# Kernel tuning notes

Measured on AMD Instinct MI355X. Metric: run time of the kernel, lower is better.

## Reference

```python
import jax, jax.numpy as jnp
import numpy as np

B, N, K, EMB, OUT = 16, 1024, 20, 1024, 40
EPS = 1e-5  # BatchNorm eps; eval mode with running_mean=0, running_var=1


def _bn(x, g, b):
    # inference-mode batchnorm (running_mean=0, running_var=1) over channel axis 1
    shp = [1] * x.ndim
    shp[1] = x.shape[1]
    inv = 1.0 / jnp.sqrt(1.0 + EPS)
    return x * inv * g.reshape(shp) + b.reshape(shp)


def _lrelu(v):
    return jnp.where(v >= 0, v, 0.2 * v)


def _knn(x, k):
    # x: (B, C, N) -> (B, N, k) indices of k nearest neighbours
    inner = -2.0 * jnp.einsum('bcn,bcm->bnm', x, x)
    xx = jnp.sum(x * x, axis=1)  # (B, N)
    pd = -xx[:, :, None] - inner - xx[:, None, :]  # negative squared distance
    return jax.lax.top_k(pd, k)[1]


def _graph_feature(x, k):
    # x: (B, C, N) -> (B, 2C, N, k) edge features [x_j - x_i, x_i]
    idx = _knn(x, k)                          # (B, N, k)
    xt = jnp.transpose(x, (0, 2, 1))          # (B, N, C)
    feat = jax.vmap(lambda pts, ind: pts[ind])(xt, idx)  # (B, N, k, C)
    ctr = xt[:, :, None, :]                   # (B, N, 1, C)
    out = jnp.concatenate([feat - ctr, jnp.broadcast_to(ctr, feat.shape)], axis=3)
    return jnp.transpose(out, (0, 3, 1, 2))   # (B, 2C, N, k)


def _local_frames(x, k):
    # x: (B, 3, N) -> (B, 6, N, k); eigh-based local frame + topk gather (no_grad in torch)
    B_, _, N_ = x.shape
    diff = jnp.transpose(x[:, :, None, :] - x[:, :, :, None], (0, 2, 1, 3))  # (B,N,3,N): y[b,i,c,j]=x[b,c,j]-x[b,c,i]
    cov = jnp.einsum('bncm,bndm->bncd', diff, diff)  # (B,N,3,3)
    _, vecs = jnp.linalg.eigh(cov)
    y = jnp.einsum('bndc,bndm->bncm', vecs, diff)    # eigvecs^T @ diff, (B,N,3,N)
    diag = jnp.transpose(jnp.diagonal(y, axis1=1, axis2=3), (0, 2, 1))  # (B,N,3) = y[b,n,:,n]
    y_sub = y - diag[:, :, :, None]
    red = jnp.sum(y_sub * y_sub, axis=2)             # (B,N,N)
    idx = jax.lax.top_k(red, k)[1]                   # (B,N,k) largest
    idxe = jnp.broadcast_to(idx[:, :, None, :], (B_, N_, 3, k))
    gy = jnp.take_along_axis(y, idxe, axis=3)
    gs = jnp.take_along_axis(y_sub, idxe, axis=3)
    x0 = jnp.concatenate([gy, gs], axis=2)           # (B,N,6,k)
    return jnp.transpose(x0, (0, 2, 1, 3))           # (B,6,N,k)


def setup_inputs() -> dict:
    key = jax.random.key(0)
    ks = jax.random.split(key, 30)
    rn = lambda k_, s, sc=0.05: jax.random.normal(k_, s, jnp.float32) * sc
    gm = lambda k_, c: 1.0 + 0.1 * jax.random.normal(k_, (c,), jnp.float32)
    bt = lambda k_, c: 0.1 * jax.random.normal(k_, (c,), jnp.float32)
    return {
        'x': jax.random.normal(ks[0], (B, 3, N), jnp.float32),
        'w1': rn(ks[1], (64, 6)),    'g1': gm(ks[2], 64),  'b1': bt(ks[3], 64),
        'w2': rn(ks[4], (64, 128)),  'g2': gm(ks[5], 64),  'b2': bt(ks[6], 64),
        'w3': rn(ks[7], (128, 128)), 'g3': gm(ks[8], 128), 'b3': bt(ks[9], 128),
        'w4': rn(ks[10], (256, 256)),'g4': gm(ks[11], 256),'b4': bt(ks[12], 256),
        'w5': rn(ks[13], (EMB, 512)),'g5': gm(ks[14], EMB),'b5': bt(ks[15], EMB),
        'lw1': rn(ks[16], (512, 2 * EMB)), 'g6': gm(ks[17], 512), 'b6': bt(ks[18], 512),
        'lw2': rn(ks[19], (256, 512)), 'lb2': bt(ks[20], 256), 'g7': gm(ks[21], 256), 'b7': bt(ks[22], 256),
        'lw3': rn(ks[23], (OUT, 256)), 'lb3': bt(ks[24], OUT),
    }


def reference(x, w1, g1, b1, w2, g2, b2, w3, g3, b3, w4, g4, b4,
              w5, g5, b5, lw1, g6, b6, lw2, lb2, g7, b7, lw3, lb3):
    x0 = jax.lax.stop_gradient(_local_frames(x, K))      # torch.no_grad block
    h = _lrelu(_bn(jnp.einsum('oc,bcnk->bonk', w1, x0), g1, b1))
    x1 = jnp.max(h, axis=-1)                              # (B,64,N)
    h = _lrelu(_bn(jnp.einsum('oc,bcnk->bonk', w2, _graph_feature(x1, K)), g2, b2))
    x2 = jnp.max(h, axis=-1)                              # (B,64,N)
    h = _lrelu(_bn(jnp.einsum('oc,bcnk->bonk', w3, _graph_feature(x2, K)), g3, b3))
    x3 = jnp.max(h, axis=-1)                              # (B,128,N)
    h = _lrelu(_bn(jnp.einsum('oc,bcnk->bonk', w4, _graph_feature(x3, K)), g4, b4))
    x4 = jnp.max(h, axis=-1)                              # (B,256,N)
    xc = jnp.concatenate([x1, x2, x3, x4], axis=1)        # (B,512,N)
    h5 = _lrelu(_bn(jnp.einsum('oc,bcn->bon', w5, xc), g5, b5))  # (B,EMB,N)
    f = jnp.concatenate([jnp.max(h5, axis=-1), jnp.mean(h5, axis=-1)], axis=1)  # (B,2*EMB)
    f = _lrelu(_bn(f @ lw1.T, g6, b6))                    # dropout = identity (eval)
    f = _lrelu(_bn(f @ lw2.T + lb2, g7, b7))
    return f @ lw3.T + lb3                                # (B,OUT)
```

## Files before the change

kernel.cpp:

```cpp
#include <hip/hip_runtime.h>
#include <hip/hip_bf16.h>
#include <math.h>

#define BB 16
#define NN 1024
#define KK 20


__device__ inline float s_sign(float a, float b) { return b >= 0.0f ? fabsf(a) : -fabsf(a); }

__device__ inline float s_lapy2(float x, float y) {
    float xa = fabsf(x), ya = fabsf(y);
    float w = fmaxf(xa, ya), z = fminf(xa, ya);
    if (z == 0.0f) return w;
    float t = z / w;
    return w * sqrtf(1.0f + t * t);
}

__device__ inline void s_lartg(float f, float g, float& c, float& s, float& r) {
    const float safmin = 1.1754943508222875e-38f;
    const float safmax = 1.0f / 1.1754943508222875e-38f;
    const float rtmin = 1.0842021724855044e-19f;
    const float rtmax = 9.2233720368547758e+18f;
    float f1 = fabsf(f), g1 = fabsf(g);
    if (g == 0.0f) { c = 1.0f; s = 0.0f; r = f; }
    else if (f == 0.0f) { c = 0.0f; s = (g >= 0.0f ? 1.0f : -1.0f); r = g1; }
    else {
        float d;
        if (f1 > rtmin && f1 < rtmax && g1 > rtmin && g1 < rtmax) {
            d = sqrtf(f * f + g * g);
            c = f1 / d;
            r = (f >= 0.0f ? d : -d);
        } else {
            float u = fminf(safmax, fmaxf(safmin, fmaxf(f1, g1)));
            float fs = f / u, gs = g / u;
            d = sqrtf(fs * fs + gs * gs);
            c = fabsf(fs) / d;
            r = (f >= 0.0f ? d : -d);
            r = r * u;
        }
        s = g / r;
    }
}

__device__ void s_laev2(float a, float b, float cc, float& rt1, float& rt2,
                        float& cs1, float& sn1) {
    float sm = a + cc;
    float df = a - cc;
    float adf = fabsf(df);
    float tb = b + b;
    float ab = fabsf(tb);
    float acmx, acmn;
    if (fabsf(a) > fabsf(cc)) { acmx = a; acmn = cc; } else { acmx = cc; acmn = a; }
    float rt;
    if (adf > ab) { float t = ab / adf; rt = adf * sqrtf(1.0f + t * t); }
    else if (adf < ab) { float t = adf / ab; rt = ab * sqrtf(1.0f + t * t); }
    else rt = ab * sqrtf(2.0f);
    int sgn1;
    if (sm < 0.0f) { rt1 = 0.5f * (sm - rt); sgn1 = -1; rt2 = (acmx / rt1) * acmn - (b / rt1) * b; }
    else if (sm > 0.0f) { rt1 = 0.5f * (sm + rt); sgn1 = 1; rt2 = (acmx / rt1) * acmn - (b / rt1) * b; }
    else { rt1 = 0.5f * rt; rt2 = -0.5f * rt; sgn1 = 1; }
    float cs; int sgn2;
    if (df >= 0.0f) { cs = df + rt; sgn2 = 1; } else { cs = df - rt; sgn2 = -1; }
    float acs = fabsf(cs);
    if (acs > ab) {
        float ct = -tb / cs;
        sn1 = 1.0f / sqrtf(1.0f + ct * ct);
        cs1 = ct * sn1;
    } else {
        if (ab == 0.0f) { cs1 = 1.0f; sn1 = 0.0f; }
        else {
            float tn = -cs / tb;
            cs1 = 1.0f / sqrtf(1.0f + tn * tn);
            sn1 = tn * cs1;
        }
    }
    if (sgn1 == sgn2) { float tn = cs1; cs1 = -sn1; sn1 = tn; }
}

__device__ void ssteqr3(float* d, float* e, float z[4][4]) {
    const float EPS = 5.9604644775390625e-08f;
    const float EPS2 = 3.5527136788005009e-15f;
    const float SAFMIN = 1.1754943508222875e-38f;
    const float SAFMAX = 1.0f / 1.1754943508222875e-38f;
    const float SSFMAX = sqrtf(SAFMAX) / 3.0f;
    const float SSFMIN = sqrtf(SAFMIN) / EPS2;
    const int n = 3;
    float cwork[4], swork[4];
    int nmaxit = n * 30, jtot = 0;
    int l1 = 1, nm1 = n - 1;
    int l, lsv, lend, lendsv, m, iscale;
    float anorm = 0.0f, p, g, r, c, s, f, b, rt1, rt2;
    int i, j, mm;
    float tst, sc, temp, ct, st;

L10:
    if (l1 > n) goto L160;
    if (l1 > 1) e[l1 - 1] = 0.0f;
    if (l1 <= nm1) {
        for (m = l1; m <= nm1; ++m) {
            tst = fabsf(e[m]);
            if (tst == 0.0f) goto L30;
            if (tst <= (sqrtf(fabsf(d[m])) * sqrtf(fabsf(d[m + 1]))) * EPS) { e[m] = 0.0f; goto L30; }
        }
    }
    m = n;
L30:
    l = l1; lsv = l; lend = m; lendsv = lend; l1 = m + 1;
    if (lend == l) goto L10;
    anorm = 0.0f;
    for (i = l; i <= lend; ++i) anorm = fmaxf(anorm, fabsf(d[i]));
    for (i = l; i <= lend - 1; ++i) anorm = fmaxf(anorm, fabsf(e[i]));
    iscale = 0;
    if (anorm == 0.0f) goto L10;
    if (anorm > SSFMAX) {
        iscale = 1; sc = SSFMAX / anorm;
        for (i = l; i <= lend; ++i) d[i] *= sc;
        for (i = l; i <= lend - 1; ++i) e[i] *= sc;
    } else if (anorm < SSFMIN) {
        iscale = 2; sc = SSFMIN / anorm;
        for (i = l; i <= lend; ++i) d[i] *= sc;
        for (i = l; i <= lend - 1; ++i) e[i] *= sc;
    }
    if (fabsf(d[lend]) < fabsf(d[l])) { lend = lsv; l = lendsv; }
    if (lend > l) {
L40:
        if (l != lend) {
            for (m = l; m <= lend - 1; ++m) {
                tst = fabsf(e[m]); tst = tst * tst;
                if (tst <= (EPS2 * fabsf(d[m])) * fabsf(d[m + 1]) + SAFMIN) goto L60;
            }
        }
        m = lend;
L60:
        if (m < lend) e[m] = 0.0f;
        p = d[l];
        if (m == l) goto L80;
        if (m == l + 1) {
            s_laev2(d[l], e[l], d[l + 1], rt1, rt2, c, s);
            for (i = 1; i <= n; ++i) {
                temp = z[i][l + 1];
                z[i][l + 1] = c * temp - s * z[i][l];
                z[i][l] = s * temp + c * z[i][l];
            }
            d[l] = rt1; d[l + 1] = rt2; e[l] = 0.0f;
            l += 2;
            if (l <= lend) goto L40;
            goto L140;
        }
        if (jtot == nmaxit) goto L140;
        ++jtot;
        g = (d[l + 1] - p) / (2.0f * e[l]);
        r = s_lapy2(g, 1.0f);
        g = d[m] - p + (e[l] / (g + s_sign(r, g)));
        s = 1.0f; c = 1.0f; p = 0.0f;
        for (i = m - 1; i >= l; --i) {
            f = s * e[i]; b = c * e[i];
            s_lartg(g, f, c, s, r);
            if (i != m - 1) e[i + 1] = r;
            g = d[i + 1] - p;
            r = (d[i] - g) * s + 2.0f * c * b;
            p = s * r;
            d[i + 1] = g + p;
            g = c * r - b;
            cwork[i] = c; swork[i] = -s;
        }
        mm = m - l + 1;
        for (j = mm - 1; j >= 1; --j) {
            ct = cwork[l + j - 1]; st = swork[l + j - 1];
            for (i = 1; i <= n; ++i) {
                temp = z[i][l + j];
                z[i][l + j] = ct * temp - st * z[i][l + j - 1];
                z[i][l + j - 1] = st * temp + ct * z[i][l + j - 1];
            }
        }
        d[l] = d[l] - p;
        e[l] = g;
        goto L40;
L80:
        d[l] = p;
        l = l + 1;
        if (l <= lend) goto L40;
        goto L140;
    } else {
L90:
        if (l != lend) {
            for (m = l; m >= lend + 1; --m) {
                tst = fabsf(e[m - 1]); tst = tst * tst;
                if (tst <= (EPS2 * fabsf(d[m])) * fabsf(d[m - 1]) + SAFMIN) goto L110;
            }
        }
        m = lend;
L110:
    if (m > lend) e[m - 1] = 0.0f;
        p = d[l];
        if (m == l) goto L130;
        if (m == l - 1) {
            s_laev2(d[l - 1], e[l - 1], d[l], rt1, rt2, c, s);
            for (i = 1; i <= n; ++i) {
                temp = z[i][l];
                z[i][l] = c * temp - s * z[i][l - 1];
                z[i][l - 1] = s * temp + c * z[i][l - 1];
            }
            d[l - 1] = rt1; d[l] = rt2; e[l - 1] = 0.0f;
            l -= 2;
            if (l >= lend) goto L90;
            goto L140;
        }
        if (jtot == nmaxit) goto L140;
        ++jtot;
        g = (d[l - 1] - p) / (2.0f * e[l - 1]);
        r = s_lapy2(g, 1.0f);
        g = d[m] - p + (e[l - 1] / (g + s_sign(r, g)));
        s = 1.0f; c = 1.0f; p = 0.0f;
        for (i = m; i <= l - 1; ++i) {
            f = s * e[i]; b = c * e[i];
            s_lartg(g, f, c, s, r);
            if (i != m) e[i - 1] = r;
            g = d[i] - p;
            r = (d[i + 1] - g) * s + 2.0f * c * b;
            p = s * r;
            d[i] = g + p;
            g = c * r - b;
            cwork[i] = c; swork[i] = s;
        }
        mm = l - m + 1;
        for (j = 1; j <= mm - 1; ++j) {
            ct = cwork[m + j - 1]; st = swork[m + j - 1];
            for (i = 1; i <= n; ++i) {
                temp = z[i][m + j];
                z[i][m + j] = ct * temp - st * z[i][m + j - 1];
                z[i][m + j - 1] = st * temp + ct * z[i][m + j - 1];
            }
        }
        d[l] = d[l] - p;
        e[l - 1] = g;
        goto L90;
L130:
        d[l] = p;
        l = l - 1;
        if (l >= lend) goto L90;
        goto L140;
    }
L140:
    if (iscale == 1) {
        sc = anorm / SSFMAX;
        for (i = lsv; i <= lendsv; ++i) d[i] *= sc;
        for (i = lsv; i <= lendsv - 1; ++i) e[i] *= sc;
    } else if (iscale == 2) {
        sc = anorm / SSFMIN;
        for (i = lsv; i <= lendsv; ++i) d[i] *= sc;
        for (i = lsv; i <= lendsv - 1; ++i) e[i] *= sc;
    }
    if (jtot < nmaxit) goto L10;
    return;
L160:
    for (int ii = 2; ii <= n; ++ii) {
        i = ii - 1; int k = i;
        p = d[i];
        for (j = ii; j <= n; ++j) {
            if (d[j] < p) { k = j; p = d[j]; }
        }
        if (k != i) {
            d[k] = d[i]; d[i] = p;
            for (int rr = 1; rr <= n; ++rr) { float t = z[rr][i]; z[rr][i] = z[rr][k]; z[rr][k] = t; }
        }
    }
}

__device__ void eigh3f(const float A[3][3], float vecs[3][3]) {
    float a00 = A[0][0], a10 = A[1][0], a20 = A[2][0];
    float a11 = A[1][1], a21 = A[2][1], a22 = A[2][2];
    float d[4], e[4], tau1, v2 = 0.0f, beta;
    float alpha = a10, xnorm = fabsf(a20);
    if (xnorm == 0.0f) {
        tau1 = 0.0f; beta = alpha;
    } else {
        beta = -s_sign(s_lapy2(alpha, xnorm), alpha);
        tau1 = (beta - alpha) / beta;
        v2 = a20 * (1.0f / (alpha - beta));
    }
    e[1] = beta;
    if (tau1 != 0.0f) {
        float w0 = tau1 * (a11 + a21 * v2);
        float w1 = tau1 * (a21 + a22 * v2);
        float al = -0.5f * tau1 * (w0 + w1 * v2);
        w0 += al; w1 += al * v2;
        a11 = a11 - w0 - w0;
        a21 = a21 - v2 * w0 - w1;
        a22 = a22 - v2 * w1 - w1 * v2;
    }
    e[2] = a21;
    d[1] = a00; d[2] = a11; d[3] = a22;
    float z[4][4];
    for (int i = 1; i <= 3; ++i)
        for (int j = 1; j <= 3; ++j) z[i][j] = (i == j) ? 1.0f : 0.0f;
    ssteqr3(d, e, z);
    if (tau1 != 0.0f) {
        for (int j = 1; j <= 3; ++j) {
            float sum = z[2][j] + v2 * z[3][j];
            z[2][j] -= tau1 * sum;
            z[3][j] -= tau1 * v2 * sum;
        }
    }
    for (int c = 0; c < 3; ++c) {
        vecs[0][c] = z[1][c + 1];
        vecs[1][c] = z[2][c + 1];
        vecs[2][c] = z[3][c + 1];
    }
}

__global__ __launch_bounds__(256) void transpose_w2_kernel(const float* __restrict__ w,
                                                           float* __restrict__ wp,
                                                           int R, int C) {
    int i = blockIdx.x * 256 + threadIdx.x;
    if (i < R * C) {
        int r = i / C, c = i % C;
        int pc = c >> 1, k = c & 1;
        wp[((size_t)pc * R + r) * 2 + k] = w[i];
    }
}

__global__ __launch_bounds__(256) void transpose_w4_kernel(const float* __restrict__ w,
                                                           float* __restrict__ wq,
                                                           int R, int C) {
    int i = blockIdx.x * 256 + threadIdx.x;
    if (i < R * C) {
        int r = i / C, c = i % C;
        int qc = c >> 2, k = c & 3;
        wq[((size_t)qc * R + r) * 4 + k] = w[i];
    }
}

__global__ __launch_bounds__(256) void transpose_w_kernel(const float* __restrict__ w,
                                                          float* __restrict__ wt,
                                                          int R, int C) {
    int i = blockIdx.x * 256 + threadIdx.x;
    if (i < R * C) {
        int r = i / C, c = i % C;
        wt[(size_t)c * R + r] = w[i];
    }
}

template <int C>
__global__ __launch_bounds__(256) void transpose_x_kernel(const double* __restrict__ xt,
                                                          double* __restrict__ xtc) {
    __shared__ double tile[32][33];
    const int ctiles = C / 32, ntiles = NN / 32;
    int id = blockIdx.x;
    int b = id / (ctiles * ntiles);
    int rem = id % (ctiles * ntiles);
    int ct = rem / ntiles, nt = rem % ntiles;
    int c0 = ct * 32, n0 = nt * 32;
    int tc = threadIdx.x & 31, tr = threadIdx.x >> 5;
    for (int rr = tr; rr < 32; rr += 8)
        tile[rr][tc] = xt[((size_t)b * NN + n0 + rr) * C + c0 + tc];
    __syncthreads();
    for (int rr = tr; rr < 32; rr += 8)
        xtc[((size_t)b * C + c0 + rr) * NN + n0 + tc] = tile[tc][rr];
}

__global__ __launch_bounds__(256) void cov6_kernel(const float* __restrict__ x,
                                                   double* __restrict__ cov6) {
    int bn = blockIdx.x;
    int b = bn >> 10, n = bn & 1023;
    __shared__ double covp[6][4];
    const float* xb = x + (size_t)b * 3 * NN;
    float cx = xb[n], cy = xb[NN + n], cz = xb[2 * NN + n];
    double c00 = 0, c01 = 0, c02 = 0, c11 = 0, c12 = 0, c22 = 0;
    for (int m = threadIdx.x; m < NN; m += 256) {
        double dx = (double)xb[m] - (double)cx;
        double dy = (double)xb[NN + m] - (double)cy;
        double dz = (double)xb[2 * NN + m] - (double)cz;
        c00 += dx * dx; c01 += dx * dy; c02 += dx * dz;
        c11 += dy * dy; c12 += dy * dz; c22 += dz * dz;
    }
    for (int off = 32; off; off >>= 1) {
        c00 += __shfl_down(c00, off); c01 += __shfl_down(c01, off);
        c02 += __shfl_down(c02, off); c11 += __shfl_down(c11, off);
        c12 += __shfl_down(c12, off); c22 += __shfl_down(c22, off);
    }
    int lane = threadIdx.x & 63, wv = threadIdx.x >> 6;
    if (lane == 0) {
        covp[0][wv] = c00; covp[1][wv] = c01; covp[2][wv] = c02;
        covp[3][wv] = c11; covp[4][wv] = c12; covp[5][wv] = c22;
    }
    __syncthreads();
    if (threadIdx.x == 0) {
        double* outp = cov6 + (size_t)bn * 6;
        outp[0] = covp[0][0] + covp[0][1] + covp[0][2] + covp[0][3];
        outp[1] = covp[1][0] + covp[1][1] + covp[1][2] + covp[1][3];
        outp[2] = covp[2][0] + covp[2][1] + covp[2][2] + covp[2][3];
        outp[3] = covp[3][0] + covp[3][1] + covp[3][2] + covp[3][3];
        outp[4] = covp[4][0] + covp[4][1] + covp[4][2] + covp[4][3];
        outp[5] = covp[5][0] + covp[5][1] + covp[5][2] + covp[5][3];
    }
}

__global__ __launch_bounds__(256) void eigh_kernel(const double* __restrict__ cov6,
                                                   double* __restrict__ vecsg) {
    int i = blockIdx.x * 256 + threadIdx.x;
    if (i < BB * NN) {
        const double* s = cov6 + (size_t)i * 6;
        double s00 = s[0], s01 = s[1], s02 = s[2], s11 = s[3], s12 = s[4], s22 = s[5];
        float A[3][3];
        A[0][0] = (float)s00; A[0][1] = (float)s01; A[0][2] = (float)s02;
        A[1][0] = (float)s01; A[1][1] = (float)s11; A[1][2] = (float)s12;
        A[2][0] = (float)s02; A[2][1] = (float)s12; A[2][2] = (float)s22;
        float V[3][3];
        eigh3f(A, V);
        double* vp = vecsg + (size_t)i * 9;
        for (int dd = 0; dd < 3; ++dd)
            for (int cc2 = 0; cc2 < 3; ++cc2) vp[dd * 3 + cc2] = (double)V[dd][cc2];
    }
}

__global__ __launch_bounds__(256) void lf_rest_kernel(
    const float* __restrict__ x, const double* __restrict__ vecsg,
    const float* __restrict__ w1, const float* __restrict__ g1, const float* __restrict__ b1,
    float* __restrict__ x1, double* __restrict__ x1t) {
    int bn = blockIdx.x;
    int b = bn >> 10, n = bn & 1023;
    __shared__ float xs[3][NN];
    __shared__ double red[NN];
    __shared__ int sel[KK];
    __shared__ double ysel[3][KK];

    const float* xb = x + (size_t)b * 3 * NN;
    for (int t = threadIdx.x; t < 3 * NN; t += 256) xs[t >> 10][t & 1023] = xb[t];
    __syncthreads();

    float cx = xs[0][n], cy = xs[1][n], cz = xs[2][n];
    const double* vp = vecsg + (size_t)bn * 9;
    double v00 = vp[0], v01 = vp[1], v02 = vp[2];
    double v10 = vp[3], v11 = vp[4], v12 = vp[5];
    double v20 = vp[6], v21 = vp[7], v22 = vp[8];
    for (int m = threadIdx.x; m < NN; m += 256) {
        double dx = (double)xs[0][m] - (double)cx;
        double dy = (double)xs[1][m] - (double)cy;
        double dz = (double)xs[2][m] - (double)cz;
        double y0 = v00 * dx + v10 * dy + v20 * dz;
        double y1 = v01 * dx + v11 * dy + v21 * dz;
        double y2 = v02 * dx + v12 * dy + v22 * dz;
        red[m] = y0 * y0 + y1 * y1 + y2 * y2;
    }
    __syncthreads();
    if (threadIdx.x < 64) {
        double v[16];
#pragma unroll
        for (int j = 0; j < 16; ++j) v[j] = red[threadIdx.x + 64 * j];
        for (int it = 0; it < KK; ++it) {
            double bv = v[0]; int bj = 0;
#pragma unroll
            for (int j = 1; j < 16; ++j) {
                if (v[j] > bv) { bv = v[j]; bj = j; }
            }
            int bm = (bj << 6) + threadIdx.x;
            for (int off2 = 1; off2 < 64; off2 <<= 1) {
                double ov = __shfl_xor(bv, off2);
                int om = __shfl_xor(bm, off2);
                if (ov > bv || (ov == bv && om < bm)) { bv = ov; bm = om; }
            }
            int cj = bm >> 6;
            bool mine = (bm & 63) == (int)threadIdx.x;
#pragma unroll
            for (int j = 0; j < 16; ++j)
                if (j == cj && mine) v[j] = -1.0;
            if (threadIdx.x == 0) sel[it] = bm;
        }
    }
    __syncthreads();
    if (threadIdx.x < KK) {
        int m = sel[threadIdx.x];
        double dx = (double)xs[0][m] - (double)cx;
        double dy = (double)xs[1][m] - (double)cy;
        double dz = (double)xs[2][m] - (double)cz;
        ysel[0][threadIdx.x] = v00 * dx + v10 * dy + v20 * dz;
        ysel[1][threadIdx.x] = v01 * dx + v11 * dy + v21 * dz;
        ysel[2][threadIdx.x] = v02 * dx + v12 * dy + v22 * dz;
    }
    __syncthreads();
    if (threadIdx.x < 64) {
        int o = threadIdx.x;
        double wr0 = w1[o * 6 + 0], wr1 = w1[o * 6 + 1], wr2 = w1[o * 6 + 2];
        double wr3 = w1[o * 6 + 3], wr4 = w1[o * 6 + 4], wr5 = w1[o * 6 + 5];
        const double inv = 1.0 / sqrt(1.0 + 1e-5);
        double go = g1[o], bo = b1[o];
        double best = -INFINITY;
        for (int j = 0; j < KK; ++j) {
            double y0 = ysel[0][j], y1 = ysel[1][j], y2 = ysel[2][j];
            double a = wr0 * y0 + wr1 * y1 + wr2 * y2 + wr3 * y0 + wr4 * y1 + wr5 * y2;
            double h = a * inv * go + bo;
            h = h >= 0.0 ? h : 0.2 * h;
            best = fmax(best, h);
        }
        x1[((size_t)b * 64 + o) * NN + n] = (float)best;
        x1t[((size_t)(b * NN + n)) * 64 + o] = best;
    }
}

template <int C>
__global__ __launch_bounds__(256) void xx_kernel(const double* __restrict__ xtc, double* __restrict__ xx) {
    int i = blockIdx.x * 256 + threadIdx.x;
    if (i < BB * NN) {
        int b = i >> 10, m = i & 1023;
        const double* col = xtc + (size_t)b * C * NN + m;
        double s = 0.0;
        for (int c = 0; c < C; ++c) s = fma(col[(size_t)c * NN], col[(size_t)c * NN], s);
        xx[i] = s;
    }
}

template <int C>
__global__ __launch_bounds__(256) void knn_kernel(const double* __restrict__ xt,
                                                  const double* __restrict__ xtc,
                                                  const double* __restrict__ xx,
                                                  int* __restrict__ idx) {
    int b = blockIdx.x >> 8;
    int n0 = (blockIdx.x & 255) << 2;
    __shared__ alignas(16) double ctr[4][C];
    __shared__ alignas(16) double pd[4][NN];
    int tid = threadIdx.x;

    const double* qbase = xt + (size_t)(b * NN + n0) * C;
    for (int t = tid; t < 4 * C; t += 256) (&ctr[0][0])[t] = qbase[t];
    __syncthreads();

    double xxq[4];
#pragma unroll
    for (int q = 0; q < 4; ++q) xxq[q] = xx[b * NN + n0 + q];

    {
        const double* colb = xtc + (size_t)b * C * NN;
        double acc[4][4];
#pragma unroll
        for (int q = 0; q < 4; ++q)
#pragma unroll
            for (int mm = 0; mm < 4; ++mm) acc[q][mm] = 0.0;
#pragma unroll 4
        for (int c = 0; c < C; ++c) {
            const double* col = colb + (size_t)c * NN;
            double rv0 = col[tid];
            double rv1 = col[tid + 256];
            double rv2 = col[tid + 512];
            double rv3 = col[tid + 768];
            double cq0 = ctr[0][c], cq1 = ctr[1][c], cq2 = ctr[2][c], cq3 = ctr[3][c];
            acc[0][0] = fma(cq0, rv0, acc[0][0]);
            acc[0][1] = fma(cq0, rv1, acc[0][1]);
            acc[0][2] = fma(cq0, rv2, acc[0][2]);
            acc[0][3] = fma(cq0, rv3, acc[0][3]);
            acc[1][0] = fma(cq1, rv0, acc[1][0]);
            acc[1][1] = fma(cq1, rv1, acc[1][1]);
            acc[1][2] = fma(cq1, rv2, acc[1][2]);
            acc[1][3] = fma(cq1, rv3, acc[1][3]);
            acc[2][0] = fma(cq2, rv0, acc[2][0]);
            acc[2][1] = fma(cq2, rv1, acc[2][1]);
            acc[2][2] = fma(cq2, rv2, acc[2][2]);
            acc[2][3] = fma(cq2, rv3, acc[2][3]);
            acc[3][0] = fma(cq3, rv0, acc[3][0]);
            acc[3][1] = fma(cq3, rv1, acc[3][1]);
            acc[3][2] = fma(cq3, rv2, acc[3][2]);
            acc[3][3] = fma(cq3, rv3, acc[3][3]);
        }
#pragma unroll
        for (int mm = 0; mm < 4; ++mm) {
            int m = tid + 256 * mm;
            double xm = xx[b * NN + m];
#pragma unroll
            for (int q = 0; q < 4; ++q)
                pd[q][m] = (-xxq[q] + 2.0 * acc[q][mm]) - xm;
        }
    }
    __syncthreads();

    int wv = tid >> 6, lane = tid & 63;
    double v[16];
#pragma unroll
    for (int j = 0; j < 16; ++j) v[j] = pd[wv][lane + 64 * j];
    int* out = idx + (size_t)(b * NN + n0 + wv) * KK;
    for (int it = 0; it < KK; ++it) {
        double bv = v[0]; int bj = 0;
#pragma unroll
        for (int j = 1; j < 16; ++j) {
            if (v[j] > bv) { bv = v[j]; bj = j; }
        }
        int bm = (bj << 6) + lane;
        for (int off = 1; off < 64; off <<= 1) {
            double ov = __shfl_xor(bv, off);
            int om = __shfl_xor(bm, off);
            if (ov > bv || (ov == bv && om < bm)) { bv = ov; bm = om; }
        }
        int cj = bm >> 6;
        bool mine = (bm & 63) == lane;
#pragma unroll
        for (int j = 0; j < 16; ++j)
            if (j == cj && mine) v[j] = -INFINITY;
        if (lane == 0) out[it] = bm;
    }
}

template <int CIN, int COUT, int P>
__global__ __launch_bounds__(256) void conv_kernel(
    const double* __restrict__ xint, const int* __restrict__ idx,
    const float* __restrict__ wp, const float* __restrict__ g, const float* __restrict__ bbias,
    float* __restrict__ xout, double* __restrict__ xoutt) {
    const int bpb = NN / P;
    int b = blockIdx.x / bpb;
    int n0 = (blockIdx.x % bpb) * P;
    int tid = threadIdx.x;
    int o = tid % COUT, p = tid / COUT;
    int n = n0 + p;

    __shared__ alignas(16) double ctr[P][CIN];
    __shared__ alignas(16) double dif[P][KK][CIN];
    __shared__ int midx[P][KK];

    const double* qbase = xint + (size_t)(b * NN + n0) * CIN;
    for (int t = tid; t < P * CIN; t += 256) (&ctr[0][0])[t] = qbase[t];
    for (int t = tid; t < P * KK; t += 256)
        (&midx[0][0])[t] = idx[(size_t)(b * NN + n0 + t / KK) * KK + (t % KK)];
    __syncthreads();
    for (int t = tid; t < P * KK * CIN; t += 256) {
        int p2 = t / (KK * CIN);
        int rem = t % (KK * CIN);
        int j = rem / CIN, c = rem % CIN;
        dif[p2][j][c] = xint[(size_t)(b * NN + midx[p2][j]) * CIN + c] - ctr[p2][c];
    }
    __syncthreads();

    const double inv = 1.0 / sqrt(1.0 + 1e-5);
    const float2* wpo = reinterpret_cast<const float2*>(wp) + o;
    double ct2 = 0.0;
#pragma unroll 4
    for (int c2 = 0; c2 < CIN / 2; ++c2) {
        float2 wv = wpo[(size_t)(CIN / 2 + c2) * COUT];
        double2 cv = *reinterpret_cast<const double2*>(&ctr[p][2 * c2]);
        ct2 = fma((double)wv.x, cv.x, ct2);
        ct2 = fma((double)wv.y, cv.y, ct2);
    }
    double acc[KK];
#pragma unroll
    for (int j = 0; j < KK; ++j) acc[j] = 0.0;
    for (int c2 = 0; c2 < CIN / 2; ++c2) {
        float2 wv = wpo[(size_t)c2 * COUT];
        double wx = (double)wv.x, wy = (double)wv.y;
#pragma unroll
        for (int j = 0; j < KK; ++j) {
            double2 dv = *reinterpret_cast<const double2*>(&dif[p][j][2 * c2]);
            acc[j] = fma(wx, dv.x, acc[j]);
            acc[j] = fma(wy, dv.y, acc[j]);
        }
    }
    double go = g[o], bo = bbias[o];
    double best = -INFINITY;
#pragma unroll
    for (int j = 0; j < KK; ++j) {
        double h = (acc[j] + ct2) * inv * go + bo;
        h = h >= 0.0 ? h : 0.2 * h;
        best = fmax(best, h);
    }
    xout[((size_t)b * COUT + o) * NN + n] = (float)best;
    if (xoutt) xoutt[(size_t)(b * NN + n) * COUT + o] = best;
}

__global__ __launch_bounds__(256) void gemm_ab4_kernel(
    const double* __restrict__ x3t, const float* __restrict__ wq,
    float* __restrict__ AB) {
    int b = blockIdx.x >> 8;
    int n0 = (blockIdx.x & 255) << 2;
    int o = threadIdx.x;
    __shared__ alignas(16) float xr[4][128];
    for (int t = threadIdx.x; t < 4 * 128; t += 256)
        xr[t >> 7][t & 127] = (float)x3t[((size_t)(b * NN + n0 + (t >> 7))) * 128 + (t & 127)];
    __syncthreads();
    const float4* wqc = reinterpret_cast<const float4*>(wq) + o;
    float accA[4], accB[4];
#pragma unroll
    for (int p = 0; p < 4; ++p) { accA[p] = 0.f; accB[p] = 0.f; }
    for (int qc = 0; qc < 32; ++qc) {
        float4 wv = wqc[(size_t)qc * 256];
#pragma unroll
        for (int p = 0; p < 4; ++p) {
            float4 xv = *reinterpret_cast<const float4*>(&xr[p][4 * qc]);
            accA[p] = fmaf(wv.x, xv.x, accA[p]); accA[p] = fmaf(wv.y, xv.y, accA[p]);
            accA[p] = fmaf(wv.z, xv.z, accA[p]); accA[p] = fmaf(wv.w, xv.w, accA[p]);
        }
    }
    for (int qc = 32; qc < 64; ++qc) {
        float4 wv = wqc[(size_t)qc * 256];
#pragma unroll
        for (int p = 0; p < 4; ++p) {
            float4 xv = *reinterpret_cast<const float4*>(&xr[p][4 * (qc - 32)]);
            accB[p] = fmaf(wv.x, xv.x, accB[p]); accB[p] = fmaf(wv.y, xv.y, accB[p]);
            accB[p] = fmaf(wv.z, xv.z, accB[p]); accB[p] = fmaf(wv.w, xv.w, accB[p]);
        }
    }
#pragma unroll
    for (int p = 0; p < 4; ++p) {
        float* row = AB + ((size_t)(b * NN + n0 + p)) * 512;
        row[o] = accA[p];
        row[256 + o] = accB[p];
    }
}

__global__ __launch_bounds__(256) void epi4_kernel(
    const float* __restrict__ AB, const int* __restrict__ idx,
    const float* __restrict__ g, const float* __restrict__ bbias,
    float* __restrict__ x4b) {
    int b = blockIdx.x >> 8;
    int n0 = (blockIdx.x & 255) << 2;
    int o = threadIdx.x;
    __shared__ int midx[4][KK];
    for (int t = threadIdx.x; t < 4 * KK; t += 256)
        midx[t / KK][t % KK] = idx[(size_t)(b * NN + n0 + t / KK) * KK + (t % KK)];
    __syncthreads();
    const float inv = (float)(1.0 / sqrt(1.0 + 1e-5));
    float s = inv * g[o];
    float bo = bbias[o];
#pragma unroll
    for (int p = 0; p < 4; ++p) {
        const float* ABn = AB + ((size_t)(b * NN + n0 + p)) * 512;
        float base = ABn[256 + o] - ABn[o];
        float best = -INFINITY;
        for (int j = 0; j < KK; ++j) {
            float aj = AB[((size_t)(b * NN + midx[p][j])) * 512 + o];
            float h = fmaf(aj + base, s, bo);
            h = h >= 0.f ? h : 0.2f * h;
            best = fmaxf(best, h);
        }
        x4b[((size_t)b * 256 + o) * NN + n0 + p] = best;
    }
}

__global__ __launch_bounds__(256) void gemm5_kernel(
    const float* __restrict__ x1, const float* __restrict__ x2,
    const float* __restrict__ x3, const float* __restrict__ x4,
    const float* __restrict__ w5t, const float* __restrict__ g5, const float* __restrict__ b5,
    float* __restrict__ pmax, float* __restrict__ psum) {
    int ot = blockIdx.x, nt = blockIdx.y, b = blockIdx.z;
    int o0 = ot * 128, n0 = nt * 128;
    __shared__ alignas(16) float Wt[16][132];
    __shared__ alignas(16) float Xt[16][132];
    __shared__ float rmax[128][17];
    __shared__ float rsum[128][17];
    float acc[8][8];
#pragma unroll
    for (int i = 0; i < 8; ++i)
#pragma unroll
        for (int j = 0; j < 8; ++j) acc[i][j] = 0.f;
    int tx = threadIdx.x & 15;
    int ty = threadIdx.x >> 4;
    int ka = threadIdx.x >> 5;
    int qa = threadIdx.x & 31;

    float4 wreg0, wreg1, xreg0, xreg1;

    {
        wreg0 = *reinterpret_cast<const float4*>(&w5t[(size_t)(ka)*1024 + o0 + 4 * qa]);
        wreg1 = *reinterpret_cast<const float4*>(&w5t[(size_t)(ka + 8) * 1024 + o0 + 4 * qa]);
#pragma unroll
        for (int r = 0; r < 2; ++r) {
            int c = ka + 8 * r;
            const float* src; int coff, CC;
            if (c < 64) { src = x1; coff = c; CC = 64; }
            else { src = x2; coff = c - 64; CC = 64; }
            float4 v = *reinterpret_cast<const float4*>(&src[((size_t)b * CC + coff) * NN + n0 + 4 * qa]);
            if (r == 0) xreg0 = v; else xreg1 = v;
        }
        *reinterpret_cast<float4*>(&Wt[ka][4 * qa]) = wreg0;
        *reinterpret_cast<float4*>(&Wt[ka + 8][4 * qa]) = wreg1;
        *reinterpret_cast<float4*>(&Xt[ka][4 * qa]) = xreg0;
        *reinterpret_cast<float4*>(&Xt[ka + 8][4 * qa]) = xreg1;
    }
    __syncthreads();

    for (int kk = 0; kk < 512; kk += 16) {
        bool more = (kk + 16) < 512;
        if (more) {
            int kk2 = kk + 16;
            wreg0 = *reinterpret_cast<const float4*>(&w5t[(size_t)(kk2 + ka) * 1024 + o0 + 4 * qa]);
            wreg1 = *reinterpret_cast<const float4*>(&w5t[(size_t)(kk2 + ka + 8) * 1024 + o0 + 4 * qa]);
#pragma unroll
            for (int r = 0; r < 2; ++r) {
                int c = kk2 + ka + 8 * r;
                const float* src; int coff, CC;
                if (c < 64) { src = x1; coff = c; CC = 64; }
                else if (c < 128) { src = x2; coff = c - 64; CC = 64; }
                else if (c < 256) { src = x3; coff = c - 128; CC = 128; }
                else { src = x4; coff = c - 256; CC = 256; }
                float4 v = *reinterpret_cast<const float4*>(&src[((size_t)b * CC + coff) * NN + n0 + 4 * qa]);
                if (r == 0) xreg0 = v; else xreg1 = v;
            }
        }
#pragma unroll
        for (int k = 0; k < 16; ++k) {
            float4 w0 = *reinterpret_cast<const float4*>(&Wt[k][ty * 4]);
            float4 w1 = *reinterpret_cast<const float4*>(&Wt[k][64 + ty * 4]);
            float4 xa = *reinterpret_cast<const float4*>(&Xt[k][tx * 4]);
            float4 xb2 = *reinterpret_cast<const float4*>(&Xt[k][64 + tx * 4]);
            float wv[8] = {w0.x, w0.y, w0.z, w0.w, w1.x, w1.y, w1.z, w1.w};
            float xv[8] = {xa.x, xa.y, xa.z, xa.w, xb2.x, xb2.y, xb2.z, xb2.w};
#pragma unroll
            for (int i = 0; i < 8; ++i)
#pragma unroll
                for (int j = 0; j < 8; ++j) acc[i][j] += wv[i] * xv[j];
        }
        __syncthreads();
        if (more) {
            *reinterpret_cast<float4*>(&Wt[ka][4 * qa]) = wreg0;
            *reinterpret_cast<float4*>(&Wt[ka + 8][4 * qa]) = wreg1;
            *reinterpret_cast<float4*>(&Xt[ka][4 * qa]) = xreg0;
            *reinterpret_cast<float4*>(&Xt[ka + 8][4 * qa]) = xreg1;
            __syncthreads();
        }
    }
    const float inv = (float)(1.0 / sqrt(1.0 + 1e-5));
#pragma unroll
    for (int i = 0; i < 8; ++i) {
        int o = (i < 4) ? (ty * 4 + i) : (64 + ty * 4 + (i - 4));
        float go = g5[o0 + o], bo = b5[o0 + o];
        float mx = -INFINITY, sm = 0.f;
#pragma unroll
        for (int j = 0; j < 8; ++j) {
            float h = acc[i][j] * inv * go + bo;
            h = h >= 0.f ? h : 0.2f * h;
            mx = fmaxf(mx, h);
            sm += h;
        }
        rmax[o][tx] = mx; rsum[o][tx] = sm;
    }
    __syncthreads();
    if (threadIdx.x < 128) {
        int o = threadIdx.x;
        float mx = -INFINITY, sm = 0.f;
        for (int t = 0; t < 16; ++t) { mx = fmaxf(mx, rmax[o][t]); sm += rsum[o][t]; }
        pmax[((size_t)b * 1024 + o0 + o) * 16 + nt] = mx;
        psum[((size_t)b * 1024 + o0 + o) * 16 + nt] = sm;
    }
}

__global__ __launch_bounds__(256) void poolfc_kernel(
    const float* __restrict__ pmax, const float* __restrict__ psum,
    const float* __restrict__ lw1, const float* __restrict__ g6, const float* __restrict__ b6,
    const float* __restrict__ lw2, const float* __restrict__ lb2,
    const float* __restrict__ g7, const float* __restrict__ b7,
    const float* __restrict__ lw3, const float* __restrict__ lb3,
    float* __restrict__ out) {
    int b = blockIdx.x;
    __shared__ float f[2048];
    __shared__ float f2[512];
    __shared__ float f3[256];
    for (int o = threadIdx.x; o < 1024; o += 256) {
        float mx = -INFINITY, sm = 0.f;
        for (int t = 0; t < 8; ++t) {
            mx = fmaxf(mx, pmax[((size_t)b * 1024 + o) * 16 + t]);
            sm += psum[((size_t)b * 1024 + o) * 16 + t];
        }
        f[o] = mx;
        f[1024 + o] = sm * (1.0f / 1024.0f);
    }
    __syncthreads();
    const float inv = (float)(1.0 / sqrt(1.0 + 1e-5));
    for (int o = threadIdx.x; o < 512; o += 256) {
        const float* wr = lw1 + (size_t)o * 2048;
        float acc = 0.f;
        for (int c = 0; c < 2048; ++c) acc += wr[c] * f[c];
        float h = acc * inv * g6[o] + b6[o];
        f2[o] = h >= 0.f ? h : 0.2f * h;
    }
    __syncthreads();
    for (int o = threadIdx.x; o < 256; o += 256) {
        const float* wr = lw2 + (size_t)o * 512;
        float acc = 0.f;
        for (int c = 0; c < 512; ++c) acc += wr[c] * f2[c];
        acc += lb2[o];
        float h = acc * inv * g7[o] + b7[o];
        f3[o] = h >= 0.f ? h : 0.2f * h;
    }
    __syncthreads();
    if (threadIdx.x < 40) {
        int o = threadIdx.x;
        const float* wr = lw3 + (size_t)o * 256;
        float acc = 0.f;
        for (int c = 0; c < 256; ++c) acc += wr[c] * f3[c];
        out[b * 40 + o] = acc + lb3[o];
    }
}

extern "C" void kernel_launch(void* const* d_in, const int* in_sizes, int n_in,
                              void* d_out, int out_size, void* d_ws, size_t ws_size,
                              hipStream_t stream) {
    const float* x   = (const float*)d_in[0];
    const float* w1  = (const float*)d_in[1];
    const float* g1  = (const float*)d_in[2];
    const float* b1  = (const float*)d_in[3];
    const float* w2  = (const float*)d_in[4];
    const float* g2  = (const float*)d_in[5];
    const float* b2  = (const float*)d_in[6];
    const float* w3  = (const float*)d_in[7];
    const float* g3  = (const float*)d_in[8];
    const float* b3  = (const float*)d_in[9];
    const float* w4  = (const float*)d_in[10];
    const float* g4  = (const float*)d_in[11];
    const float* b4  = (const float*)d_in[12];
    const float* w5  = (const float*)d_in[13];
    const float* g5  = (const float*)d_in[14];
    const float* b5  = (const float*)d_in[15];
    const float* lw1 = (const float*)d_in[16];
    const float* g6  = (const float*)d_in[17];
    const float* b6  = (const float*)d_in[18];
    const float* lw2 = (const float*)d_in[19];
    const float* lb2 = (const float*)d_in[20];
    const float* g7  = (const float*)d_in[21];
    const float* b7  = (const float*)d_in[22];
    const float* lw3 = (const float*)d_in[23];
    const float* lb3 = (const float*)d_in[24];

    float* ws = (float*)d_ws;
    size_t off = 0;
    float* x1b  = ws + off; off += (size_t)BB * 64 * NN;
    float* x2b  = ws + off; off += (size_t)BB * 64 * NN;
    float* x3b  = ws + off; off += (size_t)BB * 128 * NN;
    float* x4b  = ws + off; off += (size_t)BB * 256 * NN;
    float* pmax = ws + off; off += (size_t)BB * 1024 * 16;
    float* psum = ws + off; off += (size_t)BB * 1024 * 16;
    int*   idxb = (int*)(ws + off); off += (size_t)BB * NN * KK;
    float* w2t  = ws + off; off += (size_t)64 * 128;
    float* w3t  = ws + off; off += (size_t)128 * 128;
    float* w4t  = ws + off; off += (size_t)256 * 256;
    float* w5t  = ws + off; off += (size_t)512 * 1024;
    float* ab4  = ws + off; off += (size_t)BB * NN * 512;
    off = (off + 3) & ~(size_t)3;
    double* x1t = (double*)(ws + off); off += (size_t)BB * NN * 64 * 2;
    double* x2t = (double*)(ws + off); off += (size_t)BB * NN * 64 * 2;
    double* x3t = (double*)(ws + off); off += (size_t)BB * NN * 128 * 2;
    double* x1c = (double*)(ws + off); off += (size_t)BB * 64 * NN * 2;
    double* x2c = (double*)(ws + off); off += (size_t)BB * 64 * NN * 2;
    double* x3c = (double*)(ws + off); off += (size_t)BB * 128 * NN * 2;
    double* xxd = (double*)(ws + off); off += (size_t)BB * NN * 2;
    double* cov6g = (double*)(ws + off); off += (size_t)BB * NN * 6 * 2;
    double* vecsg = (double*)(ws + off); off += (size_t)BB * NN * 9 * 2;

    dim3 blk(256);
    transpose_w2_kernel<<<dim3((64 * 128 + 255) / 256), blk, 0, stream>>>(w2, w2t, 64, 128);
    transpose_w2_kernel<<<dim3((128 * 128 + 255) / 256), blk, 0, stream>>>(w3, w3t, 128, 128);
    transpose_w4_kernel<<<dim3((256 * 256 + 255) / 256), blk, 0, stream>>>(w4, w4t, 256, 256);
    transpose_w_kernel<<<dim3((1024 * 512 + 255) / 256), blk, 0, stream>>>(w5, w5t, 1024, 512);

    cov6_kernel<<<dim3(BB * NN), blk, 0, stream>>>(x, cov6g);
    eigh_kernel<<<dim3(BB * NN / 256), blk, 0, stream>>>(cov6g, vecsg);
    lf_rest_kernel<<<dim3(BB * NN), blk, 0, stream>>>(x, vecsg, w1, g1, b1, x1b, x1t);

    transpose_x_kernel<64><<<dim3(BB * 2 * 32), blk, 0, stream>>>(x1t, x1c);
    xx_kernel<64><<<dim3(BB * NN / 256), blk, 0, stream>>>(x1c, xxd);
    knn_kernel<64><<<dim3(BB * NN / 4), blk, 0, stream>>>(x1t, x1c, xxd, idxb);
    conv_kernel<64, 64, 4><<<dim3(BB * NN / 4), blk, 0, stream>>>(x1t, idxb, w2t, g2, b2, x2b, x2t);
    transpose_x_kernel<64><<<dim3(BB * 2 * 32), blk, 0, stream>>>(x2t, x2c);
    xx_kernel<64><<<dim3(BB * NN / 256), blk, 0, stream>>>(x2c, xxd);
    knn_kernel<64><<<dim3(BB * NN / 4), blk, 0, stream>>>(x2t, x2c, xxd, idxb);
    conv_kernel<64, 128, 2><<<dim3(BB * NN / 2), blk, 0, stream>>>(x2t, idxb, w3t, g3, b3, x3b, x3t);
    transpose_x_kernel<128><<<dim3(BB * 4 * 32), blk, 0, stream>>>(x3t, x3c);
    xx_kernel<128><<<dim3(BB * NN / 256), blk, 0, stream>>>(x3c, xxd);
    knn_kernel<128><<<dim3(BB * NN / 4), blk, 0, stream>>>(x3t, x3c, xxd, idxb);
    gemm_ab4_kernel<<<dim3(BB * NN / 4), blk, 0, stream>>>(x3t, w4t, ab4);
    epi4_kernel<<<dim3(BB * NN / 4), blk, 0, stream>>>(ab4, idxb, g4, b4, x4b);
    gemm5_kernel<<<dim3(8, 8, BB), blk, 0, stream>>>(x1b, x2b, x3b, x4b, w5t, g5, b5, pmax, psum);
    poolfc_kernel<<<dim3(BB), blk, 0, stream>>>(pmax, psum, lw1, g6, b6, lw2, lb2, g7, b7, lw3, lb3,
                                                (float*)d_out);
}
```

Before: 1.760 ms.

## Retile knn kernel to eight queries per 512-thread block

```diff
diff --git a/kernel.cpp b/kernel.cpp
--- a/kernel.cpp
+++ b/kernel.cpp
@@ -512,71 +512,55 @@
 }
 
 template <int C>
-__global__ __launch_bounds__(256) void knn_kernel(const double* __restrict__ xt,
+__global__ __launch_bounds__(512) void knn_kernel(const double* __restrict__ xt,
                                                   const double* __restrict__ xtc,
                                                   const double* __restrict__ xx,
                                                   int* __restrict__ idx) {
-    int b = blockIdx.x >> 8;
-    int n0 = (blockIdx.x & 255) << 2;
-    __shared__ alignas(16) double ctr[4][C];
-    __shared__ alignas(16) double pd[4][NN];
+    int b = blockIdx.x >> 7;
+    int n0 = (blockIdx.x & 127) << 3;
+    __shared__ alignas(16) double ctr[8][C];
+    __shared__ alignas(16) double pdh[8][512];
+    __shared__ double xxqs[8];
     int tid = threadIdx.x;
 
     const double* qbase = xt + (size_t)(b * NN + n0) * C;
-    for (int t = tid; t < 4 * C; t += 256) (&ctr[0][0])[t] = qbase[t];
-    __syncthreads();
-
-    double xxq[4];
-#pragma unroll
-    for (int q = 0; q < 4; ++q) xxq[q] = xx[b * NN + n0 + q];
-
-    {
-        const double* colb = xtc + (size_t)b * C * NN;
-        double acc[4][4];
-#pragma unroll
-        for (int q = 0; q < 4; ++q)
-#pragma unroll
-            for (int mm = 0; mm < 4; ++mm) acc[q][mm] = 0.0;
+    for (int t = tid; t < 8 * C; t += 512) (&ctr[0][0])[t] = qbase[t];
+    if (tid < 8) xxqs[tid] = xx[b * NN + n0 + tid];
+    __syncthreads();
+
+    int wv = tid >> 6, lane = tid & 63;
+    double v[16];
+    const double* colb = xtc + (size_t)b * C * NN;
+
+    for (int h = 0; h < 2; ++h) {
+        int m = h * 512 + tid;
+        double acc[8];
+#pragma unroll
+        for (int q = 0; q < 8; ++q) acc[q] = 0.0;
 #pragma unroll 4
         for (int c = 0; c < C; ++c) {
-            const double* col = colb + (size_t)c * NN;
-            double rv0 = col[tid];
-            double rv1 = col[tid + 256];
-            double rv2 = col[tid + 512];
-            double rv3 = col[tid + 768];
-            double cq0 = ctr[0][c], cq1 = ctr[1][c], cq2 = ctr[2][c], cq3 = ctr[3][c];
-            acc[0][0] = fma(cq0, rv0, acc[0][0]);
-            acc[0][1] = fma(cq0, rv1, acc[0][1]);
-            acc[0][2] = fma(cq0, rv2, acc[0][2]);
-            acc[0][3] = fma(cq0, rv3, acc[0][3]);
-            acc[1][0] = fma(cq1, rv0, acc[1][0]);
-            acc[1][1] = fma(cq1, rv1, acc[1][1]);
-            acc[1][2] = fma(cq1, rv2, acc[1][2]);
-            acc[1][3] = fma(cq1, rv3, acc[1][3]);
-            acc[2][0] = fma(cq2, rv0, acc[2][0]);
-            acc[2][1] = fma(cq2, rv1, acc[2][1]);
-            acc[2][2] = fma(cq2, rv2, acc[2][2]);
-            acc[2][3] = fma(cq2, rv3, acc[2][3]);
-            acc[3][0] = fma(cq3, rv0, acc[3][0]);
-            acc[3][1] = fma(cq3, rv1, acc[3][1]);
-            acc[3][2] = fma(cq3, rv2, acc[3][2]);
-            acc[3][3] = fma(cq3, rv3, acc[3][3]);
-        }
-#pragma unroll
-        for (int mm = 0; mm < 4; ++mm) {
-            int m = tid + 256 * mm;
-            double xm = xx[b * NN + m];
-#pragma unroll
-            for (int q = 0; q < 4; ++q)
-                pd[q][m] = (-xxq[q] + 2.0 * acc[q][mm]) - xm;
-        }
-    }
-    __syncthreads();
-
-    int wv = tid >> 6, lane = tid & 63;
-    double v[16];
-#pragma unroll
-    for (int j = 0; j < 16; ++j) v[j] = pd[wv][lane + 64 * j];
+            double rv = colb[(size_t)c * NN + m];
+            double c0 = ctr[0][c], c1 = ctr[1][c], c2 = ctr[2][c], c3 = ctr[3][c];
+            double c4 = ctr[4][c], c5 = ctr[5][c], c6 = ctr[6][c], c7 = ctr[7][c];
+            acc[0] = fma(c0, rv, acc[0]);
+            acc[1] = fma(c1, rv, acc[1]);
+            acc[2] = fma(c2, rv, acc[2]);
+            acc[3] = fma(c3, rv, acc[3]);
+            acc[4] = fma(c4, rv, acc[4]);
+            acc[5] = fma(c5, rv, acc[5]);
+            acc[6] = fma(c6, rv, acc[6]);
+            acc[7] = fma(c7, rv, acc[7]);
+        }
+        double xm = xx[b * NN + m];
+        if (h == 1) __syncthreads();
+#pragma unroll
+        for (int q = 0; q < 8; ++q)
+            pdh[q][tid] = (-xxqs[q] + 2.0 * acc[q]) - xm;
+        __syncthreads();
+#pragma unroll
+        for (int j = 0; j < 8; ++j) v[8 * h + j] = pdh[wv][lane + 64 * j];
+    }
+
     int* out = idx + (size_t)(b * NN + n0 + wv) * KK;
     for (int it = 0; it < KK; ++it) {
         double bv = v[0]; int bj = 0;
@@ -942,6 +926,7 @@
     double* vecsg = (double*)(ws + off); off += (size_t)BB * NN * 9 * 2;
 
     dim3 blk(256);
+    dim3 blk512(512);
     transpose_w2_kernel<<<dim3((64 * 128 + 255) / 256), blk, 0, stream>>>(w2, w2t, 64, 128);
     transpose_w2_kernel<<<dim3((128 * 128 + 255) / 256), blk, 0, stream>>>(w3, w3t, 128, 128);
     transpose_w4_kernel<<<dim3((256 * 256 + 255) / 256), blk, 0, stream>>>(w4, w4t, 256, 256);
@@ -953,15 +938,15 @@
 
     transpose_x_kernel<64><<<dim3(BB * 2 * 32), blk, 0, stream>>>(x1t, x1c);
     xx_kernel<64><<<dim3(BB * NN / 256), blk, 0, stream>>>(x1c, xxd);
-    knn_kernel<64><<<dim3(BB * NN / 4), blk, 0, stream>>>(x1t, x1c, xxd, idxb);
+    knn_kernel<64><<<dim3(BB * NN / 8), blk512, 0, stream>>>(x1t, x1c, xxd, idxb);
     conv_kernel<64, 64, 4><<<dim3(BB * NN / 4), blk, 0, stream>>>(x1t, idxb, w2t, g2, b2, x2b, x2t);
     transpose_x_kernel<64><<<dim3(BB * 2 * 32), blk, 0, stream>>>(x2t, x2c);
     xx_kernel<64><<<dim3(BB * NN / 256), blk, 0, stream>>>(x2c, xxd);
-    knn_kernel<64><<<dim3(BB * NN / 4), blk, 0, stream>>>(x2t, x2c, xxd, idxb);
+    knn_kernel<64><<<dim3(BB * NN / 8), blk512, 0, stream>>>(x2t, x2c, xxd, idxb);
     conv_kernel<64, 128, 2><<<dim3(BB * NN / 2), blk, 0, stream>>>(x2t, idxb, w3t, g3, b3, x3b, x3t);
     transpose_x_kernel<128><<<dim3(BB * 4 * 32), blk, 0, stream>>>(x3t, x3c);
     xx_kernel<128><<<dim3(BB * NN / 256), blk, 0, stream>>>(x3c, xxd);
-    knn_kernel<128><<<dim3(BB * NN / 4), blk, 0, stream>>>(x3t, x3c, xxd, idxb);
+    knn_kernel<128><<<dim3(BB * NN / 8), blk512, 0, stream>>>(x3t, x3c, xxd, idxb);
     gemm_ab4_kernel<<<dim3(BB * NN / 4), blk, 0, stream>>>(x3t, w4t, ab4);
     epi4_kernel<<<dim3(BB * NN / 4), blk, 0, stream>>>(ab4, idxb, g4, b4, x4b);
     gemm5_kernel<<<dim3(8, 8, BB), blk, 0, stream>>>(x1b, x2b, x3b, x4b, w5t, g5, b5, pmax, psum);
```

Result: no change. 1.751 ms (-0.5%).
